# Optimization experiments

Hardware: AMD Instinct MI355X
Metric: run time of the kernel (lower is better)

Reference implementation:

```python
import jax, jax.numpy as jnp
import numpy as np

B, N, D, H = 2, 2048, 1024, 16
HD = D // H

def setup_inputs() -> dict:
    key = jax.random.key(0)
    ks = jax.random.split(key, 8)
    s = lambda fan_in: 1.0 / np.sqrt(fan_in)
    return {
        "x": jax.random.normal(ks[0], (B, N, D), jnp.float32),
        "coverage": jax.random.uniform(ks[1], (B, N, 1), jnp.float32),
        "w_qkv": jax.random.normal(ks[2], (D, 3 * D), jnp.float32) * s(D),
        "w_out": jax.random.normal(ks[3], (D, D), jnp.float32) * s(D),
        "b_out": jnp.zeros((D,), jnp.float32),
        "w_ce1": jax.random.normal(ks[4], (1, D // 4), jnp.float32),
        "b_ce1": jnp.zeros((D // 4,), jnp.float32),
        "w_ce2": jax.random.normal(ks[5], (D // 4, H), jnp.float32) * s(D // 4),
        "b_ce2": jnp.zeros((H,), jnp.float32),
        "w_fg1": jax.random.normal(ks[6], (D, D // 4), jnp.float32) * s(D),
        "b_fg1": jnp.zeros((D // 4,), jnp.float32),
        "w_fg2": jax.random.normal(ks[7], (D // 4, 1), jnp.float32) * s(D // 4),
        "b_fg2": jnp.zeros((1,), jnp.float32),
    }

def reference(x, coverage, w_qkv, w_out, b_out, w_ce1, b_ce1, w_ce2, b_ce2,
              w_fg1, b_fg1, w_fg2, b_fg2):
    b, n, d = x.shape
    h = w_ce2.shape[1]
    hd = d // h
    scale = hd ** -0.5
    qkv = x @ w_qkv  # (B,N,3D)
    q, k, v = jnp.split(qkv, 3, axis=-1)
    q = q.reshape(b, n, h, hd).transpose(0, 2, 1, 3)  # (B,H,N,hd)
    k = k.reshape(b, n, h, hd).transpose(0, 2, 1, 3)
    v = v.reshape(b, n, h, hd).transpose(0, 2, 1, 3)
    attn = jnp.einsum("bhnd,bhmd->bhnm", q, k) * scale  # (B,H,N,N)
    # coverage bias: MLP(1 -> D/4 -> H), broadcast over query dim
    cov = jax.nn.silu(coverage @ w_ce1 + b_ce1) @ w_ce2 + b_ce2  # (B,N,H)
    cov_bias = cov.transpose(0, 2, 1)[:, :, None, :]  # (B,H,1,N)
    # fusion gate on mean-pooled features
    x_pooled = x.mean(axis=1)  # (B,D)
    g = jax.nn.sigmoid(jax.nn.silu(x_pooled @ w_fg1 + b_fg1) @ w_fg2 + b_fg2)  # (B,1)
    g = g[:, :, None, None]  # (B,1,1,1)
    # g*(attn+bias) + (1-g)*attn == attn + g*bias (exact same math)
    attn = attn + g * cov_bias
    attn = jax.nn.softmax(attn, axis=-1)
    out = jnp.einsum("bhnm,bhmd->bhnd", attn, v)  # (B,H,N,hd)
    out = out.transpose(0, 2, 1, 3).reshape(b, n, d)
    return out @ w_out + b_out
```

## Files before the change

### kernel.cpp

```cpp
#include <hip/hip_runtime.h>
#include <math.h>

typedef __bf16 bf16_t;
typedef __bf16 bf16x8 __attribute__((ext_vector_type(8)));
typedef __bf16 bf16x4 __attribute__((ext_vector_type(4)));
typedef float f32x4 __attribute__((ext_vector_type(4)));

#define MFMA16(a, b, c) __builtin_amdgcn_mfma_f32_16x16x32_bf16((a), (b), (c), 0, 0, 0)

constexpr int Bc = 2, Nc = 2048, Dc = 1024, Hc = 16, HDc = 64;
constexpr float C1 = 0.18033688011112042f;
constexpr float LOG2E = 1.4426950408889634f;

__device__ __forceinline__ void glds16(const bf16_t* g, bf16_t* l) {
    __builtin_amdgcn_global_load_lds(
        (const __attribute__((address_space(1))) unsigned int*)g,
        (__attribute__((address_space(3))) unsigned int*)l, 16, 0, 0);
}

__device__ __forceinline__ void tr64_body(const float* __restrict__ src,
                                          bf16_t* __restrict__ dst, int R, int C,
                                          int bx, int by, bf16_t* tile, int t) {
    int r0 = by * 64, c0 = bx * 64;
    int cl = t & 63, rl = t >> 6;
#pragma unroll
    for (int p = 0; p < 16; ++p) {
        int r = p * 4 + rl;
        tile[r * 66 + cl] = (bf16_t)src[(size_t)(r0 + r) * C + c0 + cl];
    }
    __syncthreads();
#pragma unroll
    for (int p = 0; p < 16; ++p) {
        int r = p * 4 + rl;
        dst[(size_t)(c0 + r) * R + r0 + cl] = tile[cl * 66 + r];
    }
}

__global__ __launch_bounds__(256) void prep(const float* __restrict__ x,
                                            bf16_t* __restrict__ Xb,
                                            const float* __restrict__ w_qkv,
                                            bf16_t* __restrict__ Wt,
                                            const float* __restrict__ w_out,
                                            bf16_t* __restrict__ WoT,
                                            float* __restrict__ pooled,
                                            const float* __restrict__ coverage,
                                            const float* __restrict__ w_ce1,
                                            const float* __restrict__ b_ce1,
                                            const float* __restrict__ w_ce2,
                                            const float* __restrict__ b_ce2,
                                            float* __restrict__ cbias) {
    __shared__ __align__(16) float smem[8768];
    int bid = blockIdx.x, t = threadIdx.x;

    if (bid < 64) {
        float* w1s = smem;
        float* b1s = smem + 256;
        float* w2s = smem + 512;
        float* part = smem + 4608;
        int b = bid >> 5, n0 = (bid & 31) * 64;
        w1s[t] = w_ce1[t];
        b1s[t] = b_ce1[t];
        {
            float4* w2v = (float4*)w2s;
            const float4* g4 = (const float4*)w_ce2;
#pragma unroll
            for (int i = 0; i < 4; ++i) w2v[i * 256 + t] = g4[i * 256 + t];
        }
        __syncthreads();
        int wv = t >> 6, lane2 = t & 63;
        float c = coverage[b * 2048 + n0 + lane2];
        float acc[16];
#pragma unroll
        for (int hh = 0; hh < 16; ++hh) acc[hh] = 0.f;
        for (int jj = 0; jj < 64; ++jj) {
            int j = wv * 64 + jj;
            float tv = fmaf(c, w1s[j], b1s[j]);
            tv = tv / (1.0f + __expf(-tv));
#pragma unroll
            for (int hh = 0; hh < 16; ++hh)
                acc[hh] = fmaf(tv, w2s[j * 16 + hh], acc[hh]);
        }
#pragma unroll
        for (int hh = 0; hh < 16; ++hh) part[lane2 * 65 + wv * 16 + hh] = acc[hh];
        __syncthreads();
#pragma unroll
        for (int i = 0; i < 4; ++i) {
            int idx = t + i * 256;
            int nl = idx >> 4, hh = idx & 15;
            const float* pr = part + nl * 65 + hh;
            float s = pr[0] + pr[16] + pr[32] + pr[48];
            cbias[((size_t)b * 16 + hh) * 2048 + n0 + nl] = LOG2E * (s + b_ce2[hh]);
        }
    } else if (bid < 832) {
        int bb = bid - 64;
        tr64_body(w_qkv, Wt, 1024, 3072, bb % 48, bb / 48, (bf16_t*)smem, t);
    } else if (bid < 1088) {
        int bb = bid - 832;
        tr64_body(w_out, WoT, 1024, 1024, bb & 15, bb >> 4, (bf16_t*)smem, t);
    } else {
        int blk = bid - 1088;
        int b = blk >> 7;
        int rbase = blk * 16;
        int d = t * 4;
        float s0 = 0.f, s1 = 0.f, s2 = 0.f, s3 = 0.f;
        for (int rr = 0; rr < 16; ++rr) {
            size_t off = (size_t)(rbase + rr) * 1024 + d;
            float4 v = *(const float4*)(x + off);
            s0 += v.x; s1 += v.y; s2 += v.z; s3 += v.w;
            bf16x4 o = { (bf16_t)v.x, (bf16_t)v.y, (bf16_t)v.z, (bf16_t)v.w };
            *(bf16x4*)(Xb + off) = o;
        }
        atomicAdd(&pooled[b * 1024 + d + 0], s0);
        atomicAdd(&pooled[b * 1024 + d + 1], s1);
        atomicAdd(&pooled[b * 1024 + d + 2], s2);
        atomicAdd(&pooled[b * 1024 + d + 3], s3);
    }
}

__global__ __launch_bounds__(256) void qkv_gemm(const bf16_t* __restrict__ Xb,
                                                const bf16_t* __restrict__ Wt,
                                                bf16_t* __restrict__ Q,
                                                bf16_t* __restrict__ Kb,
                                                bf16_t* __restrict__ Vt,
                                                const float* __restrict__ pooled,
                                                const float* __restrict__ w_fg1,
                                                const float* __restrict__ b_fg1,
                                                const float* __restrict__ w_fg2,
                                                float* __restrict__ hacc) {
    __shared__ __align__(16) bf16_t At[2][128 * 32];
    __shared__ __align__(16) bf16_t Bt[2][128 * 32];
    int t = threadIdx.x;

    if (blockIdx.y == 24) {
        __shared__ float red[4];
        int blk = blockIdx.x;
        int b = blk >> 4, jb = (blk & 15) * 16;
        for (int jj = 0; jj < 16; ++jj) {
            int j = jb + jj;
            float p = 0.f;
#pragma unroll
            for (int i = 0; i < 4; ++i) {
                int d = t * 4 + i;
                p += pooled[b * 1024 + d] * w_fg1[d * 256 + j];
            }
#pragma unroll
            for (int off = 32; off > 0; off >>= 1) p += __shfl_down(p, off);
            if ((t & 63) == 0) red[t >> 6] = p;
            __syncthreads();
            if (t == 0) {
                float hj = (red[0] + red[1] + red[2] + red[3]) * (1.0f / 2048.0f) + b_fg1[j];
                hj = hj / (1.0f + __expf(-hj));
                atomicAdd(&hacc[b], hj * w_fg2[j]);
            }
            __syncthreads();
        }
        return;
    }

    int w = t >> 6, lane = t & 63;
    int l16 = lane & 15, quad = lane >> 4;
    int wm = w & 1, wx = w >> 1;
    int m0 = blockIdx.x * 128;
    int n0 = blockIdx.y * 128;
    f32x4 acc[4][4] = {};
    int sw = (l16 >> 2) & 3;

    int arow[2], asc[2], aoff[2];
#pragma unroll
    for (int i = 0; i < 2; ++i) {
        int fb = i * 4096 + w * 1024;
        int f = fb + lane * 16;
        int row = f >> 6;
        int ch = (f >> 4) & 3;
        arow[i] = row;
        asc[i] = ch ^ ((row >> 2) & 3);
        aoff[i] = fb >> 1;
    }
    auto stage = [&](int k0, int bf) {
#pragma unroll
        for (int i = 0; i < 2; ++i) {
            glds16(Wt + (size_t)(n0 + arow[i]) * 1024 + k0 + asc[i] * 8, At[bf] + aoff[i]);
            glds16(Xb + (size_t)(m0 + arow[i]) * 1024 + k0 + asc[i] * 8, Bt[bf] + aoff[i]);
        }
    };

    stage(0, 0);
    for (int ks = 0; ks < 32; ++ks) {
        int sel = ks & 1;
        asm volatile("s_waitcnt lgkmcnt(0)" ::: "memory");
        __builtin_amdgcn_s_barrier();
        if (ks + 1 < 32) {
            stage((ks + 1) * 32, sel ^ 1);
            asm volatile("s_waitcnt vmcnt(4)" ::: "memory");
        } else {
            asm volatile("s_waitcnt vmcnt(0)" ::: "memory");
        }
        __builtin_amdgcn_s_barrier();
        __builtin_amdgcn_sched_barrier(0);

        const bf16_t* Ab = At[sel];
        const bf16_t* Bb = Bt[sel];
        bf16x8 afr[4], bfr[4];
#pragma unroll
        for (int mi = 0; mi < 4; ++mi)
            afr[mi] = *(const bf16x8*)(Ab + (wm * 64 + mi * 16 + l16) * 32 + ((quad ^ sw) * 8));
#pragma unroll
        for (int ni = 0; ni < 4; ++ni)
            bfr[ni] = *(const bf16x8*)(Bb + (wx * 64 + ni * 16 + l16) * 32 + ((quad ^ sw) * 8));
        __builtin_amdgcn_s_setprio(1);
#pragma unroll
        for (int mi = 0; mi < 4; ++mi)
#pragma unroll
            for (int ni = 0; ni < 4; ++ni)
                acc[mi][ni] = MFMA16(afr[mi], bfr[ni], acc[mi][ni]);
        __builtin_amdgcn_s_setprio(0);
    }

    int sec = n0 >> 10;
    float scq = (sec == 0) ? C1 : 1.0f;
#pragma unroll
    for (int mi = 0; mi < 4; ++mi) {
        int gc = n0 + wm * 64 + mi * 16 + quad * 4;
        int dcol = gc & 1023;
        int h = dcol >> 6, hd = dcol & 63;
#pragma unroll
        for (int ni = 0; ni < 4; ++ni) {
            int gx = m0 + wx * 64 + ni * 16 + l16;
            int b = gx >> 11, n = gx & 2047;
            size_t bh = (size_t)(b * 16 + h);
            if (sec == 2) {
#pragma unroll
                for (int r = 0; r < 4; ++r)
                    Vt[(bh * 64 + hd + r) * 2048 + n] = (bf16_t)acc[mi][ni][r];
            } else {
                bf16x4 pk = { (bf16_t)(acc[mi][ni][0] * scq), (bf16_t)(acc[mi][ni][1] * scq),
                              (bf16_t)(acc[mi][ni][2] * scq), (bf16_t)(acc[mi][ni][3] * scq) };
                bf16_t* dst = (sec == 0 ? Q : Kb);
                *(bf16x4*)(dst + (bh * 2048 + n) * 64 + hd) = pk;
            }
        }
    }
}

__global__ __launch_bounds__(256) void attn_k(const bf16_t* __restrict__ Q,
                                              const bf16_t* __restrict__ Kb,
                                              const bf16_t* __restrict__ Vt,
                                              const float* __restrict__ cbias,
                                              const float* __restrict__ hacc,
                                              const float* __restrict__ b_fg2,
                                              bf16_t* __restrict__ O) {
    __shared__ __align__(16) bf16_t kbuf[2][64 * 64];
    __shared__ __align__(16) bf16_t vbuf[2][64 * 64];
    __shared__ __align__(16) float ball[2048];
    int t = threadIdx.x, w = t >> 6, lane = t & 63;
    int l16 = lane & 15, quad = lane >> 4;
    int id = blockIdx.x;
    int xcd = id & 7, slot = id >> 3;
    int bh = xcd * 4 + (slot >> 4);
    int xblk = slot & 15;
    int b = bh >> 4, h = bh & 15;
    int qa = xblk * 128 + w * 32;
    const bf16_t* Qh = Q + (size_t)bh * 2048 * 64;
    const bf16_t* Kh = Kb + (size_t)bh * 2048 * 64;
    const bf16_t* Vh = Vt + (size_t)bh * 64 * 2048;
    const float* bih = cbias + (size_t)bh * 2048;
    float g = 1.0f / (1.0f + __expf(-(hacc[b] + b_fg2[0])));

#pragma unroll
    for (int c = 0; c < 2; ++c) {
        float4 v = *(const float4*)(bih + c * 1024 + t * 4);
        float4 sv = { v.x * g, v.y * g, v.z * g, v.w * g };
        *(float4*)(ball + c * 1024 + t * 4) = sv;
    }

    int fb0 = w * 2048, fb1 = fb0 + 1024;
    int f0 = fb0 + lane * 16, f1 = fb1 + lane * 16;
    int krow0 = f0 >> 7, kch0 = ((f0 >> 4) & 7) ^ (krow0 & 7);
    int krow1 = f1 >> 7, kch1 = ((f1 >> 4) & 7) ^ (krow1 & 7);

    bf16x8 qf[2][2];
#pragma unroll
    for (int qt = 0; qt < 2; ++qt)
#pragma unroll
        for (int dh = 0; dh < 2; ++dh)
            qf[qt][dh] = *(const bf16x8*)(Qh + (size_t)(qa + qt * 16 + l16) * 64 + dh * 32 + quad * 8);

    f32x4 o[2][4] = {};
    f32x4 lacc[2] = {};
    bf16x8 onesb;
#pragma unroll
    for (int i = 0; i < 8; ++i) onesb[i] = (bf16_t)1.0f;
    int swl = l16 & 7;
    int qh = quad >> 1, ql = quad & 1;

    int bk0 = l16 * 64 + ((quad ^ swl) * 8);
    int bk1 = l16 * 64 + (((4 + quad) ^ swl) * 8);
    int bv0 = l16 * 64 + ql * 4 + ((qh ^ swl) * 8);
    int bv1 = l16 * 64 + ql * 4 + (((2 + qh) ^ swl) * 8);
    int bv2 = l16 * 64 + ql * 4 + (((4 + qh) ^ swl) * 8);
    int bv3 = l16 * 64 + ql * 4 + (((6 + qh) ^ swl) * 8);

    auto stage = [&](int tile_, int bf) {
        int jn = tile_ * 64;
        glds16(Kh + (size_t)(jn + krow0) * 64 + kch0 * 8, &kbuf[bf][fb0 >> 1]);
        glds16(Kh + (size_t)(jn + krow1) * 64 + kch1 * 8, &kbuf[bf][fb1 >> 1]);
        glds16(Vh + (size_t)krow0 * 2048 + jn + kch0 * 8, &vbuf[bf][fb0 >> 1]);
        glds16(Vh + (size_t)krow1 * 2048 + jn + kch1 * 8, &vbuf[bf][fb1 >> 1]);
    };

    stage(0, 0);

    for (int it = 0; it < 32; ++it) {
        int sel = it & 1, j0 = it * 64;
        asm volatile("s_waitcnt lgkmcnt(0)" ::: "memory");
        __builtin_amdgcn_s_barrier();
        if (it + 1 < 32) {
            stage(it + 1, sel ^ 1);
            asm volatile("s_waitcnt vmcnt(4)" ::: "memory");
        } else {
            asm volatile("s_waitcnt vmcnt(0)" ::: "memory");
        }
        __builtin_amdgcn_s_barrier();
        __builtin_amdgcn_sched_barrier(0);

        const bf16_t* kb = &kbuf[sel][0];
        const bf16_t* vb = &vbuf[sel][0];

        f32x4 s[2][4];
        __builtin_amdgcn_s_setprio(1);
#pragma unroll
        for (int kt = 0; kt < 4; ++kt) {
            f32x4 bi = *(const f32x4*)(ball + j0 + kt * 16 + quad * 4);
            bf16x8 kf0 = *(const bf16x8*)(kb + kt * 1024 + bk0);
            bf16x8 kf1 = *(const bf16x8*)(kb + kt * 1024 + bk1);
#pragma unroll
            for (int qt = 0; qt < 2; ++qt) {
                s[qt][kt] = MFMA16(kf0, qf[qt][0], bi);
                s[qt][kt] = MFMA16(kf1, qf[qt][1], s[qt][kt]);
            }
        }
        __builtin_amdgcn_s_setprio(0);

        bf16x8 pf[2][2];
#pragma unroll
        for (int qt = 0; qt < 2; ++qt) {
#pragma unroll
            for (int kt = 0; kt < 4; ++kt)
#pragma unroll
                for (int r = 0; r < 4; ++r)
                    s[qt][kt][r] = __builtin_amdgcn_exp2f(s[qt][kt][r]);
#pragma unroll
            for (int pv = 0; pv < 2; ++pv) {
                bf16x8 tmp;
#pragma unroll
                for (int i = 0; i < 4; ++i) {
                    tmp[i]     = (bf16_t)s[qt][2 * pv][i];
                    tmp[i + 4] = (bf16_t)s[qt][2 * pv + 1][i];
                }
                pf[qt][pv] = tmp;
            }
        }

        __builtin_amdgcn_s_setprio(1);
#pragma unroll
        for (int qt = 0; qt < 2; ++qt) {
            lacc[qt] = MFMA16(pf[qt][0], onesb, lacc[qt]);
            lacc[qt] = MFMA16(pf[qt][1], onesb, lacc[qt]);
        }
#pragma unroll
        for (int dt = 0; dt < 4; ++dt) {
            bf16x4 va0 = *(const bf16x4*)(vb + dt * 1024 + bv0);
            bf16x4 vc0 = *(const bf16x4*)(vb + dt * 1024 + bv1);
            bf16x8 vf0 = __builtin_shufflevector(va0, vc0, 0, 1, 2, 3, 4, 5, 6, 7);
            bf16x4 va1 = *(const bf16x4*)(vb + dt * 1024 + bv2);
            bf16x4 vc1 = *(const bf16x4*)(vb + dt * 1024 + bv3);
            bf16x8 vf1 = __builtin_shufflevector(va1, vc1, 0, 1, 2, 3, 4, 5, 6, 7);
#pragma unroll
            for (int qt = 0; qt < 2; ++qt) {
                o[qt][dt] = MFMA16(pf[qt][0], vf0, o[qt][dt]);
                o[qt][dt] = MFMA16(pf[qt][1], vf1, o[qt][dt]);
            }
        }
        __builtin_amdgcn_s_setprio(0);
    }

#pragma unroll
    for (int qt = 0; qt < 2; ++qt) {
        f32x4 rinv;
#pragma unroll
        for (int r = 0; r < 4; ++r) rinv[r] = 1.0f / lacc[qt][r];
#pragma unroll
        for (int dt = 0; dt < 4; ++dt)
#pragma unroll
            for (int r = 0; r < 4; ++r) {
                int row = qa + qt * 16 + quad * 4 + r;
                O[(size_t)(b * 2048 + row) * 1024 + h * 64 + dt * 16 + l16] =
                    (bf16_t)(o[qt][dt][r] * rinv[r]);
            }
    }
}

__global__ __launch_bounds__(256) void out_gemm(const bf16_t* __restrict__ A,
                                                const bf16_t* __restrict__ Wt,
                                                const float* __restrict__ bias,
                                                float* __restrict__ Cout) {
    __shared__ __align__(16) bf16_t At[128 * 32];
    __shared__ __align__(16) bf16_t Bt[128 * 32];
    int t = threadIdx.x, w = t >> 6, lane = t & 63;
    int l16 = lane & 15, quad = lane >> 4;
    int wm = w & 1, wx = w >> 1;
    int m0 = blockIdx.x * 128;
    int n0 = blockIdx.y * 128;
    f32x4 acc[4][4] = {};
    int sw = (l16 >> 2) & 3;

    for (int k0 = 0; k0 < 1024; k0 += 32) {
#pragma unroll
        for (int i = 0; i < 2; ++i) {
            int fb = i * 4096 + w * 1024;
            int f = fb + lane * 16;
            int row = f >> 6;
            int ch = (f >> 4) & 3;
            int sc = ch ^ ((row >> 2) & 3);
            glds16(Wt + (size_t)(n0 + row) * 1024 + k0 + sc * 8, At + (fb >> 1));
            glds16(A + (size_t)(m0 + row) * 1024 + k0 + sc * 8, Bt + (fb >> 1));
        }
        __syncthreads();
        bf16x8 afr[4], bfr[4];
#pragma unroll
        for (int mi = 0; mi < 4; ++mi)
            afr[mi] = *(const bf16x8*)(At + (wm * 64 + mi * 16 + l16) * 32 + ((quad ^ sw) * 8));
#pragma unroll
        for (int ni = 0; ni < 4; ++ni)
            bfr[ni] = *(const bf16x8*)(Bt + (wx * 64 + ni * 16 + l16) * 32 + ((quad ^ sw) * 8));
#pragma unroll
        for (int mi = 0; mi < 4; ++mi)
#pragma unroll
            for (int ni = 0; ni < 4; ++ni)
                acc[mi][ni] = MFMA16(afr[mi], bfr[ni], acc[mi][ni]);
        __syncthreads();
    }

#pragma unroll
    for (int mi = 0; mi < 4; ++mi) {
        int gc = n0 + wm * 64 + mi * 16 + quad * 4;
        float4 bv = *(const float4*)(bias + gc);
#pragma unroll
        for (int ni = 0; ni < 4; ++ni) {
            int gx = m0 + wx * 64 + ni * 16 + l16;
            float4 ov = { acc[mi][ni][0] + bv.x, acc[mi][ni][1] + bv.y,
                          acc[mi][ni][2] + bv.z, acc[mi][ni][3] + bv.w };
            *(float4*)(Cout + (size_t)gx * 1024 + gc) = ov;
        }
    }
}

extern "C" void kernel_launch(void* const* d_in, const int* in_sizes, int n_in,
                              void* d_out, int out_size, void* d_ws, size_t ws_size,
                              hipStream_t stream) {
    const float* x     = (const float*)d_in[0];
    const float* cov   = (const float*)d_in[1];
    const float* w_qkv = (const float*)d_in[2];
    const float* w_out = (const float*)d_in[3];
    const float* b_out = (const float*)d_in[4];
    const float* w_ce1 = (const float*)d_in[5];
    const float* b_ce1 = (const float*)d_in[6];
    const float* w_ce2 = (const float*)d_in[7];
    const float* b_ce2 = (const float*)d_in[8];
    const float* w_fg1 = (const float*)d_in[9];
    const float* b_fg1 = (const float*)d_in[10];
    const float* w_fg2 = (const float*)d_in[11];
    const float* b_fg2 = (const float*)d_in[12];

    char* ws = (char*)d_ws;
    bf16_t* Wt     = (bf16_t*)(ws);
    bf16_t* WoT    = (bf16_t*)(ws + 6291456);
    bf16_t* Xb     = (bf16_t*)(ws + 8388608);
    bf16_t* Qb     = (bf16_t*)(ws + 16777216);
    bf16_t* Kbb    = (bf16_t*)(ws + 25165824);
    bf16_t* Vt     = (bf16_t*)(ws + 33554432);
    bf16_t* Ob     = (bf16_t*)(ws + 41943040);
    float*  pooled = (float*)(ws + 50331648);
    float*  hacc   = (float*)(ws + 50339840);
    float*  biasb  = (float*)(ws + 50340096);

    hipMemsetAsync(pooled, 0, 8200, stream);
    prep<<<1344, 256, 0, stream>>>(x, Xb, w_qkv, Wt, w_out, WoT, pooled,
                                   cov, w_ce1, b_ce1, w_ce2, b_ce2, biasb);
    qkv_gemm<<<dim3(32, 25), 256, 0, stream>>>(Xb, Wt, Qb, Kbb, Vt,
                                               pooled, w_fg1, b_fg1, w_fg2, hacc);
    attn_k<<<512, 256, 0, stream>>>(Qb, Kbb, Vt, biasb, hacc, b_fg2, Ob);
    out_gemm<<<dim3(32, 8), 256, 0, stream>>>(Ob, WoT, b_out, (float*)d_out);
}
```

Baseline: 240.5 us.

## Enlarge QKV GEMM tiles to 256x256 with 8 waves and split-phase staging

The QKV projection GEMM moves from 128x128 tiles with 4 waves to 256x256 tiles with 8 waves (512 threads). Each wave now computes a 128x64 sub-tile, and the global-to-LDS staging is split into two halves that are issued between the two MFMA phases of each k-step. The goal is more data reuse per byte loaded and better overlap of loads with compute. The costs are a smaller grid (16x12 tiles plus the gate row), which is fewer blocks than the CU count, more accumulator registers, and extra barriers. The fusion-gate side task is reworked to use 8 waves.

```diff
diff --git a/kernel.cpp b/kernel.cpp
--- a/kernel.cpp
+++ b/kernel.cpp
@@ -117,38 +117,36 @@
     }
 }
 
-__global__ __launch_bounds__(256) void qkv_gemm(const bf16_t* __restrict__ Xb,
-                                                const bf16_t* __restrict__ Wt,
-                                                bf16_t* __restrict__ Q,
-                                                bf16_t* __restrict__ Kb,
-                                                bf16_t* __restrict__ Vt,
-                                                const float* __restrict__ pooled,
-                                                const float* __restrict__ w_fg1,
-                                                const float* __restrict__ b_fg1,
-                                                const float* __restrict__ w_fg2,
-                                                float* __restrict__ hacc) {
-    __shared__ __align__(16) bf16_t At[2][128 * 32];
-    __shared__ __align__(16) bf16_t Bt[2][128 * 32];
+__global__ __launch_bounds__(512, 2) void qkv_gemm(const bf16_t* __restrict__ Xb,
+                                                   const bf16_t* __restrict__ Wt,
+                                                   bf16_t* __restrict__ Q,
+                                                   bf16_t* __restrict__ Kb,
+                                                   bf16_t* __restrict__ Vt,
+                                                   const float* __restrict__ pooled,
+                                                   const float* __restrict__ w_fg1,
+                                                   const float* __restrict__ b_fg1,
+                                                   const float* __restrict__ w_fg2,
+                                                   float* __restrict__ hacc) {
+    __shared__ __align__(16) bf16_t lds[2][16384];
     int t = threadIdx.x;
 
-    if (blockIdx.y == 24) {
-        __shared__ float red[4];
+    if (blockIdx.y == 12) {
+        float* red = (float*)&lds[0][0];
         int blk = blockIdx.x;
-        int b = blk >> 4, jb = (blk & 15) * 16;
-        for (int jj = 0; jj < 16; ++jj) {
+        int b = blk >> 3, jb = (blk & 7) * 32;
+        for (int jj = 0; jj < 32; ++jj) {
             int j = jb + jj;
-            float p = 0.f;
-#pragma unroll
-            for (int i = 0; i < 4; ++i) {
-                int d = t * 4 + i;
-                p += pooled[b * 1024 + d] * w_fg1[d * 256 + j];
-            }
+            int d = t * 2;
+            float p = pooled[b * 1024 + d] * w_fg1[d * 256 + j]
+                    + pooled[b * 1024 + d + 1] * w_fg1[(d + 1) * 256 + j];
 #pragma unroll
             for (int off = 32; off > 0; off >>= 1) p += __shfl_down(p, off);
             if ((t & 63) == 0) red[t >> 6] = p;
             __syncthreads();
             if (t == 0) {
-                float hj = (red[0] + red[1] + red[2] + red[3]) * (1.0f / 2048.0f) + b_fg1[j];
+                float s = red[0] + red[1] + red[2] + red[3]
+                        + red[4] + red[5] + red[6] + red[7];
+                float hj = s * (1.0f / 2048.0f) + b_fg1[j];
                 hj = hj / (1.0f + __expf(-hj));
                 atomicAdd(&hacc[b], hj * w_fg2[j]);
             }
@@ -159,73 +157,90 @@
 
     int w = t >> 6, lane = t & 63;
     int l16 = lane & 15, quad = lane >> 4;
-    int wm = w & 1, wx = w >> 1;
-    int m0 = blockIdx.x * 128;
-    int n0 = blockIdx.y * 128;
-    f32x4 acc[4][4] = {};
+    int wm = w >> 2, wn = w & 3;
+    int m0 = blockIdx.x * 256;
+    int n0 = blockIdx.y * 256;
+    f32x4 acc[8][4] = {};
     int sw = (l16 >> 2) & 3;
-
-    int arow[2], asc[2], aoff[2];
-#pragma unroll
-    for (int i = 0; i < 2; ++i) {
-        int fb = i * 4096 + w * 1024;
-        int f = fb + lane * 16;
-        int row = f >> 6;
-        int ch = (f >> 4) & 3;
-        arow[i] = row;
-        asc[i] = ch ^ ((row >> 2) & 3);
-        aoff[i] = fb >> 1;
-    }
-    auto stage = [&](int k0, int bf) {
-#pragma unroll
-        for (int i = 0; i < 2; ++i) {
-            glds16(Wt + (size_t)(n0 + arow[i]) * 1024 + k0 + asc[i] * 8, At[bf] + aoff[i]);
-            glds16(Xb + (size_t)(m0 + arow[i]) * 1024 + k0 + asc[i] * 8, Bt[bf] + aoff[i]);
-        }
+    int cq = (quad ^ sw) * 8;
+
+    int srow[4], ssc[4], sdst[4];
+    bool sB[4];
+#pragma unroll
+    for (int j = 0; j < 4; ++j) {
+        int off = w * 4096 + j * 1024 + lane * 16;
+        bool inB = off >= 16384;
+        int o2 = off - (inB ? 16384 : 0);
+        int row = o2 >> 6;
+        int ch = (o2 >> 4) & 3;
+        srow[j] = row;
+        ssc[j] = ch ^ ((row >> 2) & 3);
+        sB[j] = inB;
+        sdst[j] = (w * 4096 + j * 1024) >> 1;
+    }
+    auto stg = [&](int j, int k0, int bf) {
+        const bf16_t* src = sB[j] ? Xb + (size_t)(m0 + srow[j]) * 1024
+                                  : Wt + (size_t)(n0 + srow[j]) * 1024;
+        glds16(src + k0 + ssc[j] * 8, &lds[bf][sdst[j]]);
     };
 
-    stage(0, 0);
+    int aB = (wm * 128 + l16) * 32 + cq;
+    int bB = 8192 + (wn * 64 + l16) * 32 + cq;
+
+    stg(0, 0, 0); stg(1, 0, 0); stg(2, 0, 0); stg(3, 0, 0);
+
+#pragma unroll 1
     for (int ks = 0; ks < 32; ++ks) {
-        int sel = ks & 1;
-        asm volatile("s_waitcnt lgkmcnt(0)" ::: "memory");
-        __builtin_amdgcn_s_barrier();
+        int cb = ks & 1, k0n = (ks + 1) * 32;
         if (ks + 1 < 32) {
-            stage((ks + 1) * 32, sel ^ 1);
-            asm volatile("s_waitcnt vmcnt(4)" ::: "memory");
+            stg(0, k0n, cb ^ 1); stg(1, k0n, cb ^ 1);
+            asm volatile("s_waitcnt vmcnt(2)" ::: "memory");
         } else {
             asm volatile("s_waitcnt vmcnt(0)" ::: "memory");
         }
         __builtin_amdgcn_s_barrier();
         __builtin_amdgcn_sched_barrier(0);
 
-        const bf16_t* Ab = At[sel];
-        const bf16_t* Bb = Bt[sel];
-        bf16x8 afr[4], bfr[4];
+        const bf16_t* L = lds[cb];
+        bf16x8 Ar[4], Br[4];
+#pragma unroll
+        for (int mi = 0; mi < 4; ++mi) Ar[mi] = *(const bf16x8*)(L + aB + mi * 512);
+#pragma unroll
+        for (int ni = 0; ni < 4; ++ni) Br[ni] = *(const bf16x8*)(L + bB + ni * 512);
+        __builtin_amdgcn_s_setprio(1);
 #pragma unroll
         for (int mi = 0; mi < 4; ++mi)
-            afr[mi] = *(const bf16x8*)(Ab + (wm * 64 + mi * 16 + l16) * 32 + ((quad ^ sw) * 8));
-#pragma unroll
-        for (int ni = 0; ni < 4; ++ni)
-            bfr[ni] = *(const bf16x8*)(Bb + (wx * 64 + ni * 16 + l16) * 32 + ((quad ^ sw) * 8));
+#pragma unroll
+            for (int ni = 0; ni < 4; ++ni)
+                acc[mi][ni] = MFMA16(Ar[mi], Br[ni], acc[mi][ni]);
+        __builtin_amdgcn_s_setprio(0);
+        __builtin_amdgcn_s_barrier();
+        __builtin_amdgcn_sched_barrier(0);
+
+        if (ks + 1 < 32) { stg(2, k0n, cb ^ 1); stg(3, k0n, cb ^ 1); }
+#pragma unroll
+        for (int mi = 0; mi < 4; ++mi) Ar[mi] = *(const bf16x8*)(L + aB + 2048 + mi * 512);
         __builtin_amdgcn_s_setprio(1);
 #pragma unroll
         for (int mi = 0; mi < 4; ++mi)
 #pragma unroll
             for (int ni = 0; ni < 4; ++ni)
-                acc[mi][ni] = MFMA16(afr[mi], bfr[ni], acc[mi][ni]);
+                acc[4 + mi][ni] = MFMA16(Ar[mi], Br[ni], acc[4 + mi][ni]);
         __builtin_amdgcn_s_setprio(0);
+        __builtin_amdgcn_s_barrier();
+        __builtin_amdgcn_sched_barrier(0);
     }
 
     int sec = n0 >> 10;
     float scq = (sec == 0) ? C1 : 1.0f;
 #pragma unroll
-    for (int mi = 0; mi < 4; ++mi) {
-        int gc = n0 + wm * 64 + mi * 16 + quad * 4;
+    for (int mi = 0; mi < 8; ++mi) {
+        int gc = n0 + wm * 128 + mi * 16 + quad * 4;
         int dcol = gc & 1023;
         int h = dcol >> 6, hd = dcol & 63;
 #pragma unroll
         for (int ni = 0; ni < 4; ++ni) {
-            int gx = m0 + wx * 64 + ni * 16 + l16;
+            int gx = m0 + wn * 64 + ni * 16 + l16;
             int b = gx >> 11, n = gx & 2047;
             size_t bh = (size_t)(b * 16 + h);
             if (sec == 2) {
@@ -487,7 +502,7 @@
     hipMemsetAsync(pooled, 0, 8200, stream);
     prep<<<1344, 256, 0, stream>>>(x, Xb, w_qkv, Wt, w_out, WoT, pooled,
                                    cov, w_ce1, b_ce1, w_ce2, b_ce2, biasb);
-    qkv_gemm<<<dim3(32, 25), 256, 0, stream>>>(Xb, Wt, Qb, Kbb, Vt,
+    qkv_gemm<<<dim3(16, 13), 512, 0, stream>>>(Xb, Wt, Qb, Kbb, Vt,
                                                pooled, w_fg1, b_fg1, w_fg2, hacc);
     attn_k<<<512, 256, 0, stream>>>(Qb, Kbb, Vt, biasb, hacc, b_fg2, Ob);
     out_gemm<<<dim3(32, 8), 256, 0, stream>>>(Ob, WoT, b_out, (float*)d_out);
```

New measurement: 228.5 us. 5.0% less time.
